# Kernel tuning notes

Hardware: AMD Instinct MI355X
Metric: run time of the kernel (lower is better)

Reference implementation:

```python
import jax, jax.numpy as jnp
import numpy as np

NUM_HEADS = 16
HIDDEN = 1152
MLP = 4304
HEAD_DIM = HIDDEN // NUM_HEADS  # 72
SEQ = 3072
LN_EPS = 1e-5


def setup_inputs() -> dict:
    key = jax.random.key(0)
    ks = jax.random.split(key, 16)
    inv = 1.0 / np.sqrt(HIDDEN)
    inv_m = 1.0 / np.sqrt(MLP)
    pos = jnp.arange(SEQ, dtype=jnp.float32)[:, None]
    freq = jnp.exp(-jnp.arange(HEAD_DIM // 2, dtype=jnp.float32) * (np.log(10000.0) / (HEAD_DIM // 2)))
    ang = pos * freq[None, :]
    return {
        "hidden_states": jax.random.normal(ks[0], (SEQ, HIDDEN), jnp.float32),
        "rope_cos": jnp.cos(ang),
        "rope_sin": jnp.sin(ang),
        "ln0_g": jnp.ones((HIDDEN,), jnp.float32),
        "ln0_b": jnp.zeros((HIDDEN,), jnp.float32),
        "ln1_g": jnp.ones((HIDDEN,), jnp.float32),
        "ln1_b": jnp.zeros((HIDDEN,), jnp.float32),
        "wqkv_w": jax.random.normal(ks[1], (3 * HIDDEN, HIDDEN), jnp.float32) * inv,
        "wqkv_b": jnp.zeros((3 * HIDDEN,), jnp.float32),
        "wo_w": jax.random.normal(ks[2], (HIDDEN, HIDDEN), jnp.float32) * inv,
        "wo_b": jnp.zeros((HIDDEN,), jnp.float32),
        "fc0_w": jax.random.normal(ks[3], (MLP, HIDDEN), jnp.float32) * inv,
        "fc0_b": jnp.zeros((MLP,), jnp.float32),
        "fc1_w": jax.random.normal(ks[4], (HIDDEN, MLP), jnp.float32) * inv_m,
        "fc1_b": jnp.zeros((HIDDEN,), jnp.float32),
    }


def _layernorm(x, g, b):
    mu = jnp.mean(x, axis=-1, keepdims=True)
    var = jnp.mean(jnp.square(x - mu), axis=-1, keepdims=True)
    return (x - mu) * jax.lax.rsqrt(var + LN_EPS) * g + b


def _apply_rope(x, cos, sin):
    # x: [S, H, Dh]; cos/sin: [S, Dh/2]
    xp = x.astype(jnp.float32).reshape(*x.shape[:-1], -1, 2)  # [S, H, Dh/2, 2]
    xr, xi = xp[..., 0], xp[..., 1]
    c = cos[:, None, :]
    s = sin[:, None, :]
    out_r = xr * c - xi * s
    out_i = xr * s + xi * c
    return jnp.stack([out_r, out_i], axis=-1).reshape(x.shape).astype(x.dtype)


def reference(hidden_states, rope_cos, rope_sin, ln0_g, ln0_b, ln1_g, ln1_b,
              wqkv_w, wqkv_b, wo_w, wo_b, fc0_w, fc0_b, fc1_w, fc1_b):
    S = hidden_states.shape[0]
    residual = hidden_states
    h = _layernorm(hidden_states, ln0_g, ln0_b)
    xqkv = (h @ wqkv_w.T + wqkv_b).reshape(S, 3, NUM_HEADS, HEAD_DIM)
    xq, xk, xv = xqkv[:, 0], xqkv[:, 1], xqkv[:, 2]
    xq = _apply_rope(xq, rope_cos, rope_sin)
    xk = _apply_rope(xk, rope_cos, rope_sin)
    scale = 1.0 / np.sqrt(HEAD_DIM)
    scores = jnp.einsum('shd,thd->hst', xq, xk) * scale  # [H, S, S]
    attn = jax.nn.softmax(scores.astype(jnp.float32), axis=-1).astype(xq.dtype)
    out = jnp.einsum('hst,thd->shd', attn, xv).reshape(S, HIDDEN)
    h = residual + (out @ wo_w.T + wo_b)
    residual = h
    h = _layernorm(h, ln1_g, ln1_b)
    h = jax.nn.gelu(h @ fc0_w.T + fc0_b, approximate=True)
    h = h @ fc1_w.T + fc1_b
    return residual + h
```

## Files before the change

kernel.cpp:

```cpp
#include <hip/hip_runtime.h>
#include <hip/hip_bf16.h>
#include <math.h>

typedef __hip_bfloat16 bf16;
typedef __attribute__((ext_vector_type(8))) short short8;
typedef __attribute__((ext_vector_type(4))) short short4v;
typedef __attribute__((ext_vector_type(4))) float f32x4;

#define SEQ 3072
#define HID 1152
#define NHEAD 16
#define HD 72
#define HDP 96
#define MLPD 4304
#define MLPP 4352

__device__ __forceinline__ void async_lds16(void* lds, const void* g) {
  __builtin_amdgcn_global_load_lds((const __attribute__((address_space(1))) void*)g,
                                   (__attribute__((address_space(3))) void*)lds,
                                   16, 0, 0);
}

__device__ __forceinline__ unsigned cvt_pk2(float a, float b) {
  unsigned r;
  asm("v_cvt_pk_bf16_f32 %0, %1, %2" : "=v"(r) : "v"(a), "v"(b));
  return r;
}

__device__ __forceinline__ float exp2a(float x) {
  float r;
  asm("v_exp_f32 %0, %1" : "=v"(r) : "v"(x));
  return r;
}

__device__ __forceinline__ float bflo(unsigned u) { return __uint_as_float(u << 16); }
__device__ __forceinline__ float bfhi(unsigned u) { return __uint_as_float(u & 0xffff0000u); }

__global__ __launch_bounds__(256) void prep_k(const float* __restrict__ hidden,
                                              const float* __restrict__ ln0g,
                                              const float* __restrict__ ln0b,
                                              const float* __restrict__ wqkv,
                                              const float* __restrict__ wo,
                                              const float* __restrict__ w0,
                                              const float* __restrict__ w1,
                                              bf16* __restrict__ ln0_o,
                                              unsigned* __restrict__ wqkv_o,
                                              unsigned* __restrict__ wo_o,
                                              unsigned* __restrict__ fc0_o,
                                              unsigned* __restrict__ fc1_o) {
  if (blockIdx.x < SEQ) {
    int row = blockIdx.x;
    const float4* xr = (const float4*)(hidden + (size_t)row * HID);
    float sum = 0.f, sq = 0.f;
    for (int c = threadIdx.x; c < HID / 4; c += 256) {
      float4 u = xr[c];
      sum += u.x + u.y + u.z + u.w;
      sq += u.x * u.x + u.y * u.y + u.z * u.z + u.w * u.w;
    }
#pragma unroll
    for (int off = 32; off > 0; off >>= 1) {
      sum += __shfl_down(sum, off, 64);
      sq += __shfl_down(sq, off, 64);
    }
    __shared__ float red[8];
    int wv = threadIdx.x >> 6;
    if ((threadIdx.x & 63) == 0) { red[wv] = sum; red[4 + wv] = sq; }
    __syncthreads();
    if (threadIdx.x == 0) {
      red[0] = red[0] + red[1] + red[2] + red[3];
      red[4] = red[4] + red[5] + red[6] + red[7];
    }
    __syncthreads();
    float mu = red[0] * (1.f / HID);
    float var = red[4] * (1.f / HID) - mu * mu;
    float inv = rsqrtf(var + 1e-5f);
    uint2* o4 = (uint2*)(ln0_o + (size_t)row * HID);
    const float4* g4 = (const float4*)ln0g;
    const float4* b4 = (const float4*)ln0b;
    for (int c = threadIdx.x; c < HID / 4; c += 256) {
      float4 u = xr[c], gg = g4[c], bb = b4[c];
      o4[c] = make_uint2(cvt_pk2((u.x - mu) * inv * gg.x + bb.x, (u.y - mu) * inv * gg.y + bb.y),
                         cvt_pk2((u.z - mu) * inv * gg.z + bb.z, (u.w - mu) * inv * gg.w + bb.w));
    }
    return;
  }
  const int n0 = 3 * HID * HID / 4;
  const int n1 = HID * HID / 4;
  const int n2 = MLPP * HID / 4;
  const int n3 = HID * MLPP / 4;
  const int total = n0 + n1 + n2 + n3;
  int nb = gridDim.x - SEQ;
  int stride = nb * blockDim.x;
  for (int i = (blockIdx.x - SEQ) * blockDim.x + threadIdx.x; i < total; i += stride) {
    if (i < n0) {
      float4 u = ((const float4*)wqkv)[i];
      ((uint2*)wqkv_o)[i] = make_uint2(cvt_pk2(u.x, u.y), cvt_pk2(u.z, u.w));
    } else if (i < n0 + n1) {
      int k = i - n0;
      float4 u = ((const float4*)wo)[k];
      ((uint2*)wo_o)[k] = make_uint2(cvt_pk2(u.x, u.y), cvt_pk2(u.z, u.w));
    } else if (i < n0 + n1 + n2) {
      int k = i - n0 - n1;
      int r = k / (HID / 4);
      uint2 w = make_uint2(0u, 0u);
      if (r < MLPD) {
        float4 u = ((const float4*)w0)[k];
        w = make_uint2(cvt_pk2(u.x, u.y), cvt_pk2(u.z, u.w));
      }
      ((uint2*)fc0_o)[k] = w;
    } else {
      int k = i - n0 - n1 - n2;
      int r = k / (MLPP / 4), c4 = k - r * (MLPP / 4);
      uint2 w = make_uint2(0u, 0u);
      if (c4 < MLPD / 4) {
        float4 u = ((const float4*)w1)[r * (MLPD / 4) + c4];
        w = make_uint2(cvt_pk2(u.x, u.y), cvt_pk2(u.z, u.w));
      }
      ((uint2*)fc1_o)[k] = w;
    }
  }
}

__global__ __launch_bounds__(256) void ln_bf_k(const bf16* __restrict__ x,
                                               const float* __restrict__ g,
                                               const float* __restrict__ b,
                                               bf16* __restrict__ o) {
  int row = blockIdx.x;
  const uint2* xr = (const uint2*)(x + (size_t)row * HID);
  float sum = 0.f, sq = 0.f;
  for (int c = threadIdx.x; c < HID / 4; c += 256) {
    uint2 u = xr[c];
    float a0 = bflo(u.x), a1 = bfhi(u.x), a2 = bflo(u.y), a3 = bfhi(u.y);
    sum += (a0 + a1) + (a2 + a3);
    sq += (a0 * a0 + a1 * a1) + (a2 * a2 + a3 * a3);
  }
#pragma unroll
  for (int off = 32; off > 0; off >>= 1) {
    sum += __shfl_down(sum, off, 64);
    sq += __shfl_down(sq, off, 64);
  }
  __shared__ float red[8];
  int wv = threadIdx.x >> 6;
  if ((threadIdx.x & 63) == 0) { red[wv] = sum; red[4 + wv] = sq; }
  __syncthreads();
  if (threadIdx.x == 0) {
    red[0] = red[0] + red[1] + red[2] + red[3];
    red[4] = red[4] + red[5] + red[6] + red[7];
  }
  __syncthreads();
  float mu = red[0] * (1.f / HID);
  float var = red[4] * (1.f / HID) - mu * mu;
  float inv = rsqrtf(var + 1e-5f);
  uint2* o4 = (uint2*)(o + (size_t)row * HID);
  const float4* g4 = (const float4*)g;
  const float4* b4 = (const float4*)b;
  for (int c = threadIdx.x; c < HID / 4; c += 256) {
    uint2 u = xr[c];
    float4 gg = g4[c], bb = b4[c];
    float a0 = bflo(u.x), a1 = bfhi(u.x), a2 = bflo(u.y), a3 = bfhi(u.y);
    o4[c] = make_uint2(cvt_pk2((a0 - mu) * inv * gg.x + bb.x, (a1 - mu) * inv * gg.y + bb.y),
                       cvt_pk2((a2 - mu) * inv * gg.z + bb.z, (a3 - mu) * inv * gg.w + bb.w));
  }
}

template <int EPI, int BN>
__global__ __launch_bounds__(256) void gemm_bf16(const bf16* __restrict__ A,
                                                 const bf16* __restrict__ Bt,
                                                 const float* __restrict__ bias, int nbias,
                                                 const float* __restrict__ resf,
                                                 const bf16* __restrict__ resb,
                                                 float* __restrict__ outf,
                                                 bf16* __restrict__ outb,
                                                 int M, int N, int K) {
  constexpr int NFR = (BN == 128) ? 4 : 2;
  __shared__ bf16 As[3][128 * 32];
  __shared__ bf16 Bs[3][BN * 32];
  const int t = threadIdx.x;
  const int l = t & 63;
  const int w = t >> 6;
  const int wr = w >> 1, wc = w & 1;
  const int lrow = l & 15;
  const int lks = (((l >> 4) ^ ((lrow >> 1) & 3)) & 3) * 8;
  const int wg = (blockIdx.x & 7) * (gridDim.x >> 3) + (blockIdx.x >> 3);
  const int gyt = M >> 7;
  const int xt = wg / gyt;
  const int yt = wg - xt * gyt;
  const int m0 = yt * 128;
  const int n0 = xt * BN;
  const int arow = t >> 2;
  const int ach = (((t & 3) ^ ((t >> 3) & 3)) & 3) * 8;

  const bf16* pa0 = &A[(size_t)(m0 + arow) * K + ach];
  const bf16* pa1 = &A[(size_t)(m0 + arow + 64) * K + ach];
  const bf16* pb0 = &Bt[(size_t)(n0 + arow) * K + ach];
  const bf16* pb1 = (BN == 128) ? &Bt[(size_t)(n0 + arow + 64) * K + ach] : pb0;
  auto STAGE = [&](int buf, int kt) {
    size_t off = (size_t)kt * 32;
    async_lds16(&As[buf][t * 8], pa0 + off);
    async_lds16(&As[buf][(256 + t) * 8], pa1 + off);
    async_lds16(&Bs[buf][t * 8], pb0 + off);
    if constexpr (BN == 128) async_lds16(&Bs[buf][(256 + t) * 8], pb1 + off);
  };

  f32x4 acc[4][NFR] = {};
  const int nkt = K >> 5;
  STAGE(0, 0);
  STAGE(1, 1);
  int bcur = 0;
  for (int kt = 0; kt < nkt; ++kt) {
    if (kt + 1 < nkt) {
      if constexpr (BN == 128)
        asm volatile("s_waitcnt vmcnt(4)" ::: "memory");
      else
        asm volatile("s_waitcnt vmcnt(3)" ::: "memory");
    } else {
      asm volatile("s_waitcnt vmcnt(0)" ::: "memory");
    }
    __builtin_amdgcn_s_barrier();
    int bn2 = bcur + 2;
    if (bn2 >= 3) bn2 -= 3;
    if (kt + 2 < nkt) STAGE(bn2, kt + 2);

    short8 af[4], bfr[NFR];
#pragma unroll
    for (int i = 0; i < 4; ++i)
      af[i] = *(const short8*)&As[bcur][(wr * 64 + i * 16 + lrow) * 32 + lks];
#pragma unroll
    for (int j = 0; j < NFR; ++j)
      bfr[j] = *(const short8*)&Bs[bcur][(wc * (BN >> 1) + j * 16 + lrow) * 32 + lks];
    __builtin_amdgcn_s_setprio(1);
#pragma unroll
    for (int i = 0; i < 4; ++i)
#pragma unroll
      for (int j = 0; j < NFR; ++j)
        acc[i][j] = __builtin_amdgcn_mfma_f32_16x16x32_bf16(af[i], bfr[j], acc[i][j], 0, 0, 0);
    __builtin_amdgcn_s_setprio(0);
    ++bcur;
    if (bcur == 3) bcur = 0;
  }

#pragma unroll
  for (int i = 0; i < 4; ++i) {
    int rowb = m0 + wr * 64 + i * 16 + (l >> 4) * 4;
#pragma unroll
    for (int j = 0; j < NFR; ++j) {
      int col = n0 + wc * (BN >> 1) + j * 16 + lrow;
      float bv = (col < nbias) ? bias[col] : 0.f;
#pragma unroll
      for (int r2 = 0; r2 < 4; ++r2) {
        size_t idx = (size_t)(rowb + r2) * N + col;
        float v = acc[i][j][r2] + bv;
        if (EPI == 0) {
          outb[idx] = __float2bfloat16(v);
        } else if (EPI == 1) {
          outb[idx] = __float2bfloat16(v + resf[idx]);
        } else if (EPI == 2) {
          float u = 0.7978845608028654f * (v + 0.044715f * v * v * v);
          u = fminf(fmaxf(u, -15.f), 15.f);
          float tt = __expf(2.f * u);
          outb[idx] = __float2bfloat16(v * tt / (tt + 1.f));
        } else {
          outf[idx] = v + __bfloat162float(resb[idx]);
        }
      }
    }
  }
}

__global__ __launch_bounds__(256) void rope_split(const bf16* __restrict__ xqkv,
                                                  const float* __restrict__ cosb,
                                                  const float* __restrict__ sinb,
                                                  bf16* __restrict__ qp,
                                                  bf16* __restrict__ kp,
                                                  bf16* __restrict__ vt) {
  __shared__ bf16 vl[64][72];
  const int t = threadIdx.x;
  const int h = blockIdx.y;
  const int s0 = blockIdx.x * 64;
  const float scale = 0.17002445f;
  for (int idx = t; idx < 64 * 48; idx += 256) {
    int sl = idx / 48, pi = idx - sl * 48;
    int srow = s0 + sl;
    size_t obase = ((size_t)h * SEQ + srow) * HDP + 2 * pi;
    if (pi < 36) {
      const bf16* xr = xqkv + (size_t)srow * (3 * HID) + h * HD + 2 * pi;
      unsigned qw = *(const unsigned*)xr;
      unsigned kw = *(const unsigned*)(xr + HID);
      float qr = bflo(qw), qi = bfhi(qw);
      float kr = bflo(kw), ki = bfhi(kw);
      float c = cosb[srow * 36 + pi], sn = sinb[srow * 36 + pi];
      *(unsigned*)&qp[obase] = cvt_pk2((qr * c - qi * sn) * scale, (qr * sn + qi * c) * scale);
      *(unsigned*)&kp[obase] = cvt_pk2(kr * c - ki * sn, kr * sn + ki * c);
    } else {
      *(unsigned*)&qp[obase] = 0u;
      *(unsigned*)&kp[obase] = 0u;
    }
  }
  for (int idx = t; idx < 64 * 72; idx += 256) {
    int sl = idx / 72, d = idx - sl * 72;
    vl[sl][d] = xqkv[(size_t)(s0 + sl) * (3 * HID) + 2 * HID + h * HD + d];
  }
  __syncthreads();
  bf16 z = __float2bfloat16(0.f);
  bf16 one = __float2bfloat16(1.f);
  for (int idx = t; idx < HDP * 64; idx += 256) {
    int d = idx / 64, sl = idx - d * 64;
    vt[((size_t)h * HDP + d) * SEQ + s0 + sl] = (d < 72) ? vl[sl][d] : ((d == 72) ? one : z);
  }
}

__global__ __launch_bounds__(256) void flash_attn(const bf16* __restrict__ q,
                                                  const bf16* __restrict__ kk,
                                                  const bf16* __restrict__ vT,
                                                  bf16* __restrict__ o) {
  __shared__ alignas(16) bf16 KV3[3 * 6144];
  __shared__ alignas(16) bf16 Pl[4][512];
  const int t = threadIdx.x;
  const int l = t & 63;
  const int w = t >> 6;
  const int g = l >> 4;
  const int lrow = l & 15;
  const int bid = blockIdx.x;
  const int kq = bid >> 3;
  const int h = (bid & 7) * 2 + (kq & 1);
  const int q0 = (kq >> 1) * 64 + w * 16;
  const int NT = SEQ / 32;

  const bf16* sbase[3];
  int smul[3];
#pragma unroll
  for (int i = 0; i < 3; ++i) {
    int s = t + i * 256;
    if (s < 384) {
      int cb = s >> 5, kv = s & 31;
      sbase[i] = kk + ((size_t)h * SEQ + kv) * HDP + cb * 8;
      smul[i] = 32 * HDP;
    } else {
      int vs = s - 384;
      int cb = vs / 96, d = vs - cb * 96;
      sbase[i] = vT + ((size_t)h * HDP + d) * SEQ + cb * 8;
      smul[i] = 32;
    }
  }
  auto STAGE = [&](int tile, int bufOff) {
#pragma unroll
    for (int i = 0; i < 3; ++i)
      async_lds16(&KV3[bufOff + (t + i * 256) * 8], sbase[i] + (size_t)tile * smul[i]);
  };

  short8 qf[3];
#pragma unroll
  for (int f = 0; f < 3; ++f)
    qf[f] = *(const short8*)&q[((size_t)h * SEQ + q0 + lrow) * HDP + f * 32 + g * 8];

  float m_r = -1e30f;
  f32x4 oa[5] = {};

  STAGE(0, 0);
  STAGE(1, 6144);
  STAGE(2, 12288);
  asm volatile("s_waitcnt vmcnt(6)" ::: "memory");
  __builtin_amdgcn_s_barrier();

  f32x4 stA[2] = {}, stB[2];
  int b0 = 0;
#pragma unroll
  for (int nf = 0; nf < 2; ++nf)
#pragma unroll
    for (int f = 0; f < 3; ++f) {
      short8 kfrag = *(const short8*)&KV3[0 + (f * 4 + g) * 256 + (nf * 16 + lrow) * 8];
      stA[nf] = __builtin_amdgcn_mfma_f32_16x16x32_bf16(kfrag, qf[f], stA[nf], 0, 0, 0);
    }

  for (int kt = 0; kt < NT - 1; ++kt) {
    int b1 = b0 + 6144;
    if (b1 == 18432) b1 = 0;
    asm volatile("s_waitcnt vmcnt(3)" ::: "memory");
    __builtin_amdgcn_s_barrier();

    stB[0] = (f32x4){0.f, 0.f, 0.f, 0.f};
    stB[1] = (f32x4){0.f, 0.f, 0.f, 0.f};
    __builtin_amdgcn_s_setprio(1);
#pragma unroll
    for (int nf = 0; nf < 2; ++nf)
#pragma unroll
      for (int f = 0; f < 3; ++f) {
        short8 kfrag = *(const short8*)&KV3[b1 + (f * 4 + g) * 256 + (nf * 16 + lrow) * 8];
        stB[nf] = __builtin_amdgcn_mfma_f32_16x16x32_bf16(kfrag, qf[f], stB[nf], 0, 0, 0);
      }
    __builtin_amdgcn_s_setprio(0);

    float pmax = fmaxf(fmaxf(fmaxf(stA[0][0], stA[0][1]), fmaxf(stA[0][2], stA[0][3])),
                       fmaxf(fmaxf(stA[1][0], stA[1][1]), fmaxf(stA[1][2], stA[1][3])));
    if (!__all(pmax - m_r <= 11.54f)) {
      float rm = pmax;
      rm = fmaxf(rm, __shfl_xor(rm, 16, 64));
      rm = fmaxf(rm, __shfl_xor(rm, 32, 64));
      float mn = fmaxf(m_r, rm);
      float alpha = exp2a(m_r - mn);
#pragma unroll
      for (int nf = 0; nf < 5; ++nf)
#pragma unroll
        for (int r = 0; r < 4; ++r) oa[nf][r] *= alpha;
      m_r = mn;
    }
#pragma unroll
    for (int nf = 0; nf < 2; ++nf)
#pragma unroll
      for (int r = 0; r < 4; ++r) stA[nf][r] = exp2a(stA[nf][r] - m_r);

#pragma unroll
    for (int nf = 0; nf < 2; ++nf) {
      uint2* dst = (uint2*)&Pl[w][(2 * nf + (g >> 1)) * 128 + lrow * 8 + (g & 1) * 4];
      *dst = make_uint2(cvt_pk2(stA[nf][0], stA[nf][1]), cvt_pk2(stA[nf][2], stA[nf][3]));
    }

    {
      short8 pa = *(const short8*)&Pl[w][g * 128 + lrow * 8];
      __builtin_amdgcn_s_setprio(1);
#pragma unroll
      for (int nf = 0; nf < 5; ++nf) {
        short8 bv = *(const short8*)&KV3[b0 + 3072 + g * 768 + (nf * 16 + lrow) * 8];
        oa[nf] = __builtin_amdgcn_mfma_f32_16x16x32_bf16(bv, pa, oa[nf], 0, 0, 0);
      }
      __builtin_amdgcn_s_setprio(0);
    }

    asm volatile("s_waitcnt lgkmcnt(0)" ::: "memory");
    __builtin_amdgcn_s_barrier();
    int s = kt + 3;
    if (s >= NT) s -= NT;
    STAGE(s, b0);
    stA[0] = stB[0];
    stA[1] = stB[1];
    b0 = b1;
  }

  {
    float pmax = fmaxf(fmaxf(fmaxf(stA[0][0], stA[0][1]), fmaxf(stA[0][2], stA[0][3])),
                       fmaxf(fmaxf(stA[1][0], stA[1][1]), fmaxf(stA[1][2], stA[1][3])));
    if (!__all(pmax - m_r <= 11.54f)) {
      float rm = pmax;
      rm = fmaxf(rm, __shfl_xor(rm, 16, 64));
      rm = fmaxf(rm, __shfl_xor(rm, 32, 64));
      float mn = fmaxf(m_r, rm);
      float alpha = exp2a(m_r - mn);
#pragma unroll
      for (int nf = 0; nf < 5; ++nf)
#pragma unroll
        for (int r = 0; r < 4; ++r) oa[nf][r] *= alpha;
      m_r = mn;
    }
#pragma unroll
    for (int nf = 0; nf < 2; ++nf)
#pragma unroll
      for (int r = 0; r < 4; ++r) stA[nf][r] = exp2a(stA[nf][r] - m_r);
#pragma unroll
    for (int nf = 0; nf < 2; ++nf) {
      uint2* dst = (uint2*)&Pl[w][(2 * nf + (g >> 1)) * 128 + lrow * 8 + (g & 1) * 4];
      *dst = make_uint2(cvt_pk2(stA[nf][0], stA[nf][1]), cvt_pk2(stA[nf][2], stA[nf][3]));
    }
    short8 pa = *(const short8*)&Pl[w][g * 128 + lrow * 8];
#pragma unroll
    for (int nf = 0; nf < 5; ++nf) {
      short8 bv = *(const short8*)&KV3[b0 + 3072 + g * 768 + (nf * 16 + lrow) * 8];
      oa[nf] = __builtin_amdgcn_mfma_f32_16x16x32_bf16(bv, pa, oa[nf], 0, 0, 0);
    }
  }

  asm volatile("s_waitcnt vmcnt(0)" ::: "memory");

  float lt = __shfl(oa[4][0], 32 + lrow, 64);
  float rcp = 1.f / lt;
  size_t obase = (size_t)(q0 + lrow) * HID + h * HD;
#pragma unroll
  for (int nf = 0; nf < 5; ++nf) {
    int d = nf * 16 + g * 4;
    if (d + 3 < HD) {
      uint2 pk = make_uint2(cvt_pk2(oa[nf][0] * rcp, oa[nf][1] * rcp),
                            cvt_pk2(oa[nf][2] * rcp, oa[nf][3] * rcp));
      *(uint2*)&o[obase + d] = pk;
    }
  }
}

extern "C" void kernel_launch(void* const* d_in, const int* in_sizes, int n_in,
                              void* d_out, int out_size, void* d_ws, size_t ws_size,
                              hipStream_t stream) {
  (void)in_sizes; (void)n_in; (void)out_size;
  const float* hidden = (const float*)d_in[0];
  const float* cosb = (const float*)d_in[1];
  const float* sinb = (const float*)d_in[2];
  const float* ln0g = (const float*)d_in[3];
  const float* ln0b = (const float*)d_in[4];
  const float* ln1g = (const float*)d_in[5];
  const float* ln1b = (const float*)d_in[6];
  const float* wqkv = (const float*)d_in[7];
  const float* bqkv = (const float*)d_in[8];
  const float* wo = (const float*)d_in[9];
  const float* bo = (const float*)d_in[10];
  const float* w0 = (const float*)d_in[11];
  const float* b0 = (const float*)d_in[12];
  const float* w1 = (const float*)d_in[13];
  const float* b1 = (const float*)d_in[14];

  char* p = (char*)d_ws;
  auto alloc = [&](size_t n) {
    char* r = p;
    p += (n + 255) & ~(size_t)255;
    return r;
  };
  bf16* wqkv_bf = (bf16*)alloc((size_t)3 * HID * HID * 2);
  bf16* wo_bf = (bf16*)alloc((size_t)HID * HID * 2);
  bf16* fc0_bf = (bf16*)alloc((size_t)MLPP * HID * 2);
  bf16* fc1_bf = (bf16*)alloc((size_t)HID * MLPP * 2);
  bf16* ln0_bf = (bf16*)alloc((size_t)SEQ * HID * 2);
  bf16* xqkv = (bf16*)alloc((size_t)SEQ * 3 * HID * 2);
  bf16* qp = (bf16*)alloc((size_t)NHEAD * SEQ * HDP * 2);
  bf16* kp = (bf16*)alloc((size_t)NHEAD * SEQ * HDP * 2);
  bf16* vt = (bf16*)alloc((size_t)NHEAD * HDP * SEQ * 2);
  bf16* attn_bf = (bf16*)alloc((size_t)SEQ * HID * 2);
  bf16* h1b = (bf16*)alloc((size_t)SEQ * HID * 2);
  bf16* ln1_bf = (bf16*)alloc((size_t)SEQ * HID * 2);
  bf16* gelu_bf = (bf16*)alloc((size_t)SEQ * MLPP * 2);
  if ((size_t)(p - (char*)d_ws) > ws_size) return;

  dim3 blk(256);
  prep_k<<<SEQ + 1024, blk, 0, stream>>>(hidden, ln0g, ln0b, wqkv, wo, w0, w1, ln0_bf,
                                         (unsigned*)wqkv_bf, (unsigned*)wo_bf,
                                         (unsigned*)fc0_bf, (unsigned*)fc1_bf);
  gemm_bf16<0, 128><<<dim3((3 * HID / 128) * (SEQ / 128)), blk, 0, stream>>>(
      ln0_bf, wqkv_bf, bqkv, 3 * HID, nullptr, nullptr, nullptr, xqkv, SEQ, 3 * HID, HID);
  rope_split<<<dim3(SEQ / 64, NHEAD), blk, 0, stream>>>(xqkv, cosb, sinb, qp, kp, vt);
  flash_attn<<<dim3(768), blk, 0, stream>>>(qp, kp, vt, attn_bf);
  gemm_bf16<1, 64><<<dim3((HID / 64) * (SEQ / 128)), blk, 0, stream>>>(
      attn_bf, wo_bf, bo, HID, hidden, nullptr, nullptr, h1b, SEQ, HID, HID);
  ln_bf_k<<<SEQ, blk, 0, stream>>>(h1b, ln1g, ln1b, ln1_bf);
  gemm_bf16<2, 128><<<dim3((MLPP / 128) * (SEQ / 128)), blk, 0, stream>>>(
      ln1_bf, fc0_bf, b0, MLPD, nullptr, nullptr, nullptr, gelu_bf, SEQ, MLPP, HID);
  gemm_bf16<3, 64><<<dim3((HID / 64) * (SEQ / 128)), blk, 0, stream>>>(
      gelu_bf, fc1_bf, b1, HID, nullptr, h1b, (float*)d_out, nullptr, SEQ, HID, MLPP);
}
```

Baseline: 339.5 us.

## Fuse RoPE and QKV head-split into the QKV GEMM epilogue

Replaces the QKV GEMM plus separate rope_split kernel with a dedicated gemm_qkv whose epilogue applies bias, rotary embedding (pairing lanes via shuffle), q scaling, and writes Q/K in padded head-major layout and V transposed directly. This removes the intermediate xqkv buffer write/read and one kernel launch. The padding columns of qp/kp and the ones/zero rows of vt are now filled by the prep kernel's grid-stride loop. The epilogue writes scattered bf16 scalars with per-element cos/sin loads, which may be less coalesced than before.

```diff
diff --git a/kernel.cpp b/kernel.cpp
--- a/kernel.cpp
+++ b/kernel.cpp
@@ -47,7 +47,10 @@
                                               unsigned* __restrict__ wqkv_o,
                                               unsigned* __restrict__ wo_o,
                                               unsigned* __restrict__ fc0_o,
-                                              unsigned* __restrict__ fc1_o) {
+                                              unsigned* __restrict__ fc1_o,
+                                              bf16* __restrict__ qp,
+                                              bf16* __restrict__ kp,
+                                              bf16* __restrict__ vt) {
   if (blockIdx.x < SEQ) {
     int row = blockIdx.x;
     const float4* xr = (const float4*)(hidden + (size_t)row * HID);
@@ -88,7 +91,10 @@
   const int n1 = HID * HID / 4;
   const int n2 = MLPP * HID / 4;
   const int n3 = HID * MLPP / 4;
-  const int total = n0 + n1 + n2 + n3;
+  const int n4 = NHEAD * SEQ * 6;
+  const int n5 = n4;
+  const int n6 = NHEAD * 24 * 768;
+  const int total = n0 + n1 + n2 + n3 + n4 + n5 + n6;
   int nb = gridDim.x - SEQ;
   int stride = nb * blockDim.x;
   for (int i = (blockIdx.x - SEQ) * blockDim.x + threadIdx.x; i < total; i += stride) {
@@ -108,7 +114,7 @@
         w = make_uint2(cvt_pk2(u.x, u.y), cvt_pk2(u.z, u.w));
       }
       ((uint2*)fc0_o)[k] = w;
-    } else {
+    } else if (i < n0 + n1 + n2 + n3) {
       int k = i - n0 - n1 - n2;
       int r = k / (MLPP / 4), c4 = k - r * (MLPP / 4);
       uint2 w = make_uint2(0u, 0u);
@@ -117,6 +123,21 @@
         w = make_uint2(cvt_pk2(u.x, u.y), cvt_pk2(u.z, u.w));
       }
       ((uint2*)fc1_o)[k] = w;
+    } else if (i < n0 + n1 + n2 + n3 + n4) {
+      int k = i - (n0 + n1 + n2 + n3);
+      int hs = k / 6, u = k - hs * 6;
+      ((uint2*)(qp + (size_t)hs * HDP + 72))[u] = make_uint2(0u, 0u);
+    } else if (i < n0 + n1 + n2 + n3 + n4 + n5) {
+      int k = i - (n0 + n1 + n2 + n3 + n4);
+      int hs = k / 6, u = k - hs * 6;
+      ((uint2*)(kp + (size_t)hs * HDP + 72))[u] = make_uint2(0u, 0u);
+    } else {
+      int k = i - (n0 + n1 + n2 + n3 + n4 + n5);
+      int hd = k / 768, s4 = k - hd * 768;
+      int d = 72 + (hd % 24);
+      int hh = hd / 24;
+      unsigned val = (d == 72) ? 0x3F803F80u : 0u;
+      ((uint2*)(vt + ((size_t)hh * HDP + d) * SEQ))[s4] = make_uint2(val, val);
     }
   }
 }
@@ -162,6 +183,7 @@
                        cvt_pk2((a2 - mu) * inv * gg.z + bb.z, (a3 - mu) * inv * gg.w + bb.w));
   }
 }
+
 
 template <int EPI, int BN>
 __global__ __launch_bounds__(256) void gemm_bf16(const bf16* __restrict__ A,
@@ -250,9 +272,7 @@
       for (int r2 = 0; r2 < 4; ++r2) {
         size_t idx = (size_t)(rowb + r2) * N + col;
         float v = acc[i][j][r2] + bv;
-        if (EPI == 0) {
-          outb[idx] = __float2bfloat16(v);
-        } else if (EPI == 1) {
+        if (EPI == 1) {
           outb[idx] = __float2bfloat16(v + resf[idx]);
         } else if (EPI == 2) {
           float u = 0.7978845608028654f * (v + 0.044715f * v * v * v);
@@ -267,45 +287,122 @@
   }
 }
 
-__global__ __launch_bounds__(256) void rope_split(const bf16* __restrict__ xqkv,
-                                                  const float* __restrict__ cosb,
-                                                  const float* __restrict__ sinb,
-                                                  bf16* __restrict__ qp,
-                                                  bf16* __restrict__ kp,
-                                                  bf16* __restrict__ vt) {
-  __shared__ bf16 vl[64][72];
+__global__ __launch_bounds__(256) void gemm_qkv(const bf16* __restrict__ A,
+                                                const bf16* __restrict__ Bt,
+                                                const float* __restrict__ bias,
+                                                const float* __restrict__ cosb,
+                                                const float* __restrict__ sinb,
+                                                bf16* __restrict__ qp,
+                                                bf16* __restrict__ kp,
+                                                bf16* __restrict__ vt) {
+  constexpr int BN = 128;
+  const int M = SEQ, N = 3 * HID, K = HID;
+  __shared__ bf16 As[3][128 * 32];
+  __shared__ bf16 Bs[3][BN * 32];
   const int t = threadIdx.x;
-  const int h = blockIdx.y;
-  const int s0 = blockIdx.x * 64;
-  const float scale = 0.17002445f;
-  for (int idx = t; idx < 64 * 48; idx += 256) {
-    int sl = idx / 48, pi = idx - sl * 48;
-    int srow = s0 + sl;
-    size_t obase = ((size_t)h * SEQ + srow) * HDP + 2 * pi;
-    if (pi < 36) {
-      const bf16* xr = xqkv + (size_t)srow * (3 * HID) + h * HD + 2 * pi;
-      unsigned qw = *(const unsigned*)xr;
-      unsigned kw = *(const unsigned*)(xr + HID);
-      float qr = bflo(qw), qi = bfhi(qw);
-      float kr = bflo(kw), ki = bfhi(kw);
-      float c = cosb[srow * 36 + pi], sn = sinb[srow * 36 + pi];
-      *(unsigned*)&qp[obase] = cvt_pk2((qr * c - qi * sn) * scale, (qr * sn + qi * c) * scale);
-      *(unsigned*)&kp[obase] = cvt_pk2(kr * c - ki * sn, kr * sn + ki * c);
+  const int l = t & 63;
+  const int w = t >> 6;
+  const int wr = w >> 1, wc = w & 1;
+  const int lrow = l & 15;
+  const int lks = (((l >> 4) ^ ((lrow >> 1) & 3)) & 3) * 8;
+  const int wg = (blockIdx.x & 7) * (gridDim.x >> 3) + (blockIdx.x >> 3);
+  const int gyt = M >> 7;
+  const int xt = wg / gyt;
+  const int yt = wg - xt * gyt;
+  const int m0 = yt * 128;
+  const int n0 = xt * BN;
+  const int arow = t >> 2;
+  const int ach = (((t & 3) ^ ((t >> 3) & 3)) & 3) * 8;
+
+  const bf16* pa0 = &A[(size_t)(m0 + arow) * K + ach];
+  const bf16* pa1 = &A[(size_t)(m0 + arow + 64) * K + ach];
+  const bf16* pb0 = &Bt[(size_t)(n0 + arow) * K + ach];
+  const bf16* pb1 = &Bt[(size_t)(n0 + arow + 64) * K + ach];
+  auto STAGE = [&](int buf, int kt) {
+    size_t off = (size_t)kt * 32;
+    async_lds16(&As[buf][t * 8], pa0 + off);
+    async_lds16(&As[buf][(256 + t) * 8], pa1 + off);
+    async_lds16(&Bs[buf][t * 8], pb0 + off);
+    async_lds16(&Bs[buf][(256 + t) * 8], pb1 + off);
+  };
+
+  f32x4 acc[4][4] = {};
+  const int nkt = K >> 5;
+  STAGE(0, 0);
+  STAGE(1, 1);
+  int bcur = 0;
+  for (int kt = 0; kt < nkt; ++kt) {
+    if (kt + 1 < nkt) {
+      asm volatile("s_waitcnt vmcnt(4)" ::: "memory");
     } else {
-      *(unsigned*)&qp[obase] = 0u;
-      *(unsigned*)&kp[obase] = 0u;
-    }
-  }
-  for (int idx = t; idx < 64 * 72; idx += 256) {
-    int sl = idx / 72, d = idx - sl * 72;
-    vl[sl][d] = xqkv[(size_t)(s0 + sl) * (3 * HID) + 2 * HID + h * HD + d];
-  }
-  __syncthreads();
-  bf16 z = __float2bfloat16(0.f);
-  bf16 one = __float2bfloat16(1.f);
-  for (int idx = t; idx < HDP * 64; idx += 256) {
-    int d = idx / 64, sl = idx - d * 64;
-    vt[((size_t)h * HDP + d) * SEQ + s0 + sl] = (d < 72) ? vl[sl][d] : ((d == 72) ? one : z);
+      asm volatile("s_waitcnt vmcnt(0)" ::: "memory");
+    }
+    __builtin_amdgcn_s_barrier();
+    int bn2 = bcur + 2;
+    if (bn2 >= 3) bn2 -= 3;
+    if (kt + 2 < nkt) STAGE(bn2, kt + 2);
+
+    short8 af[4], bfr[4];
+#pragma unroll
+    for (int i = 0; i < 4; ++i)
+      af[i] = *(const short8*)&As[bcur][(wr * 64 + i * 16 + lrow) * 32 + lks];
+#pragma unroll
+    for (int j = 0; j < 4; ++j)
+      bfr[j] = *(const short8*)&Bs[bcur][(wc * 64 + j * 16 + lrow) * 32 + lks];
+    __builtin_amdgcn_s_setprio(1);
+#pragma unroll
+    for (int i = 0; i < 4; ++i)
+#pragma unroll
+      for (int j = 0; j < 4; ++j)
+        acc[i][j] = __builtin_amdgcn_mfma_f32_16x16x32_bf16(af[i], bfr[j], acc[i][j], 0, 0, 0);
+    __builtin_amdgcn_s_setprio(0);
+    ++bcur;
+    if (bcur == 3) bcur = 0;
+  }
+
+  const float qscale = 0.17002445f;
+#pragma unroll
+  for (int i = 0; i < 4; ++i) {
+    int rowb = m0 + wr * 64 + i * 16 + (l >> 4) * 4;
+#pragma unroll
+    for (int j = 0; j < 4; ++j) {
+      int col = n0 + wc * 64 + j * 16 + lrow;
+      float bv = bias[col];
+      if (n0 < HID) {
+        int hh = col / HD, d = col - hh * HD;
+        int pi = d >> 1;
+        float sg = (d & 1) ? 1.f : -1.f;
+        size_t qb = (size_t)hh * SEQ * HDP + d;
+#pragma unroll
+        for (int r2 = 0; r2 < 4; ++r2) {
+          float vv = acc[i][j][r2] + bv;
+          float pr = __shfl_xor(vv, 1, 64);
+          int s = rowb + r2;
+          float cs = cosb[s * 36 + pi], sn = sinb[s * 36 + pi];
+          qp[qb + (size_t)s * HDP] = __float2bfloat16((vv * cs + pr * (sg * sn)) * qscale);
+        }
+      } else if (n0 < 2 * HID) {
+        int c2 = col - HID;
+        int hh = c2 / HD, d = c2 - hh * HD;
+        int pi = d >> 1;
+        float sg = (d & 1) ? 1.f : -1.f;
+        size_t kb = (size_t)hh * SEQ * HDP + d;
+#pragma unroll
+        for (int r2 = 0; r2 < 4; ++r2) {
+          float vv = acc[i][j][r2] + bv;
+          float pr = __shfl_xor(vv, 1, 64);
+          int s = rowb + r2;
+          float cs = cosb[s * 36 + pi], sn = sinb[s * 36 + pi];
+          kp[kb + (size_t)s * HDP] = __float2bfloat16(vv * cs + pr * (sg * sn));
+        }
+      } else {
+        int c2 = col - 2 * HID;
+        int hh = c2 / HD, d = c2 - hh * HD;
+        uint2 pk = make_uint2(cvt_pk2(acc[i][j][0] + bv, acc[i][j][1] + bv),
+                              cvt_pk2(acc[i][j][2] + bv, acc[i][j][3] + bv));
+        *(uint2*)&vt[((size_t)hh * HDP + d) * SEQ + rowb] = pk;
+      }
+    }
   }
 }
 
@@ -515,7 +612,6 @@
   bf16* fc0_bf = (bf16*)alloc((size_t)MLPP * HID * 2);
   bf16* fc1_bf = (bf16*)alloc((size_t)HID * MLPP * 2);
   bf16* ln0_bf = (bf16*)alloc((size_t)SEQ * HID * 2);
-  bf16* xqkv = (bf16*)alloc((size_t)SEQ * 3 * HID * 2);
   bf16* qp = (bf16*)alloc((size_t)NHEAD * SEQ * HDP * 2);
   bf16* kp = (bf16*)alloc((size_t)NHEAD * SEQ * HDP * 2);
   bf16* vt = (bf16*)alloc((size_t)NHEAD * HDP * SEQ * 2);
@@ -528,10 +624,9 @@
   dim3 blk(256);
   prep_k<<<SEQ + 1024, blk, 0, stream>>>(hidden, ln0g, ln0b, wqkv, wo, w0, w1, ln0_bf,
                                          (unsigned*)wqkv_bf, (unsigned*)wo_bf,
-                                         (unsigned*)fc0_bf, (unsigned*)fc1_bf);
-  gemm_bf16<0, 128><<<dim3((3 * HID / 128) * (SEQ / 128)), blk, 0, stream>>>(
-      ln0_bf, wqkv_bf, bqkv, 3 * HID, nullptr, nullptr, nullptr, xqkv, SEQ, 3 * HID, HID);
-  rope_split<<<dim3(SEQ / 64, NHEAD), blk, 0, stream>>>(xqkv, cosb, sinb, qp, kp, vt);
+                                         (unsigned*)fc0_bf, (unsigned*)fc1_bf, qp, kp, vt);
+  gemm_qkv<<<dim3((3 * HID / 128) * (SEQ / 128)), blk, 0, stream>>>(
+      ln0_bf, wqkv_bf, bqkv, cosb, sinb, qp, kp, vt);
   flash_attn<<<dim3(768), blk, 0, stream>>>(qp, kp, vt, attn_bf);
   gemm_bf16<1, 64><<<dim3((HID / 64) * (SEQ / 128)), blk, 0, stream>>>(
       attn_bf, wo_bf, bo, HID, hidden, nullptr, nullptr, h1b, SEQ, HID, HID);
```

New measurement: 329.1 us. 3.1% less time.
